# Kernel tuning notes

Measured on AMD Instinct MI355X. Metric: run time of the kernel, lower is better.

## Reference

```python
import math
import jax, jax.numpy as jnp
import numpy as np

B, FEAT, H, W = 4, 256, 48, 48
NH = 8
PE = 10            # pe_dim -> 3*PE = 30 positional channels
DK = FEAT // NH    # 32
DV = FEAT // NH    # 32
SCALE = 2.0 * math.pi
TEMPERATURE = 10000.0
BN_EPS = 1e-5


def pos_en_sine(h, w, num_pos_feats=PE):
    """3-axis sine positional encoding (y, x, and a constant 'o' axis) -> [3*PE, h, w]."""
    eps = 1e-6
    ones = jnp.ones((h, w), jnp.float32)
    y_embed = jnp.cumsum(ones, axis=0)
    x_embed = jnp.cumsum(ones, axis=1)
    y_embed = y_embed / (y_embed[-1:, :] + eps) * SCALE
    x_embed = x_embed / (x_embed[:, -1:] + eps) * SCALE
    o_embed = ones * SCALE  # third axis, constant when no explicit pos is given
    dim_t = jnp.arange(num_pos_feats, dtype=jnp.float32)
    dim_t = TEMPERATURE ** (2.0 * jnp.floor(dim_t / 2.0) / num_pos_feats)

    def enc(e):  # e: [h, w] -> [h, w, PE] interleaved sin/cos
        p = e[..., None] / dim_t
        return jnp.stack([jnp.sin(p[..., 0::2]), jnp.cos(p[..., 1::2])], axis=-1).reshape(h, w, num_pos_feats)

    pe = jnp.concatenate([enc(y_embed), enc(x_embed), enc(o_embed)], axis=-1)  # [h, w, 3*PE]
    return jnp.transpose(pe, (2, 0, 1))  # [3*PE, h, w]


def conv1x1(w, x):  # w: [out_c, in_c], x: [b, in_c, h, w]
    return jnp.einsum('oc,bchw->bohw', w, x)


def setup_inputs() -> dict:
    key = jax.random.key(0)
    ks = jax.random.split(key, 16)
    s = 0.02
    return {
        'q': jax.random.normal(ks[0], (B, FEAT, H, W), jnp.float32),
        'k': jax.random.normal(ks[1], (B, FEAT, H, W), jnp.float32),
        'v': jax.random.normal(ks[2], (B, FEAT, H, W), jnp.float32),
        'wq': jax.random.normal(ks[3], (NH * DK, FEAT + 3 * PE), jnp.float32) * s,
        'wk': jax.random.normal(ks[4], (NH * DK, FEAT + 3 * PE), jnp.float32) * s,
        'wv': jax.random.normal(ks[5], (NH * DV, FEAT), jnp.float32) * s,
        'wfc': jax.random.normal(ks[6], (FEAT, NH * DV), jnp.float32) * s,
        'w1': jax.random.normal(ks[7], (FEAT, FEAT), jnp.float32) * s,
        'b1': jnp.zeros((FEAT,), jnp.float32),
        'w2': jax.random.normal(ks[8], (FEAT, FEAT), jnp.float32) * s,
        'b2': jnp.zeros((FEAT,), jnp.float32),
        'gamma': jnp.ones((FEAT,), jnp.float32),
        'beta': jnp.zeros((FEAT,), jnp.float32),
    }


def reference(q, k, v, wq, wk, wv, wfc, w1, b1, w2, b2, gamma, beta):
    b, c, h, w = q.shape
    n = h * w
    pe = pos_en_sine(h, w)                                # [3*PE, h, w]
    peb = jnp.broadcast_to(pe[None], (b,) + pe.shape)
    qc = jnp.concatenate([q, peb], axis=1)                # [b, FEAT+30, h, w]
    kc = jnp.concatenate([k, peb], axis=1)
    # multi-head softmax attention over all spatial tokens
    Q = conv1x1(wq, qc).reshape(b, NH, DK, n)             # [b, nh, dk, n]
    K = conv1x1(wk, kc).reshape(b, NH, DK, n)
    V = conv1x1(wv, v).reshape(b, NH, DV, n)
    scores = jnp.einsum('bhdn,bhdm->bhnm', Q, K) / jnp.sqrt(jnp.float32(DK))
    attn = jax.nn.softmax(scores, axis=-1)                # [b, nh, n, n]
    O = jnp.einsum('bhnm,bhdm->bhdn', attn, V).reshape(b, NH * DV, h, w)
    O = conv1x1(wfc, O)                                   # [b, FEAT, h, w]
    # pointwise FFN + residual
    h1 = jax.nn.relu(conv1x1(w1, O) + b1[None, :, None, None])
    h2 = conv1x1(w2, h1) + b2[None, :, None, None]
    out = O + h2
    # BatchNorm2d (training mode: batch statistics over (b, h, w), biased var)
    mean = jnp.mean(out, axis=(0, 2, 3), keepdims=True)
    var = jnp.var(out, axis=(0, 2, 3), keepdims=True)
    out = (out - mean) / jnp.sqrt(var + BN_EPS)
    out = out * gamma[None, :, None, None] + beta[None, :, None, None]
    return out
```

## Files before the change

### kernel.cpp

```cpp
#include <hip/hip_runtime.h>
#include <hip/hip_bf16.h>

#define NTOK 2304

typedef short  short8  __attribute__((ext_vector_type(8)));
typedef unsigned short ushort8v __attribute__((ext_vector_type(8)));
typedef float  f32x4   __attribute__((ext_vector_type(4)));

static __device__ __forceinline__ unsigned short f2bfu(float f){
  __hip_bfloat16 h = __float2bfloat16(f);
  union { __hip_bfloat16 h; unsigned short u; } cv; cv.h = h; return cv.u;
}

static __device__ __forceinline__ void plane32(unsigned &a, unsigned &b){
  asm("v_permlane32_swap_b32 %0, %1" : "+v"(a), "+v"(b));
}
static __device__ __forceinline__ void plane16(unsigned &a, unsigned &b){
  asm("v_permlane16_swap_b32 %0, %1" : "+v"(a), "+v"(b));
}
static __device__ __forceinline__ short8 xpose_p(f32x4 sa, f32x4 sb){
  unsigned x0, x1, y0, y1;
  asm("v_cvt_pk_bf16_f32 %0, %1, %2" : "=v"(x0) : "v"(sa[0]), "v"(sa[1]));
  asm("v_cvt_pk_bf16_f32 %0, %1, %2" : "=v"(x1) : "v"(sa[2]), "v"(sa[3]));
  asm("v_cvt_pk_bf16_f32 %0, %1, %2" : "=v"(y0) : "v"(sb[0]), "v"(sb[1]));
  asm("v_cvt_pk_bf16_f32 %0, %1, %2" : "=v"(y1) : "v"(sb[2]), "v"(sb[3]));
  plane32(x0, y0);
  plane32(x1, y1);
  plane16(x0, y0);
  plane16(x1, y1);
  union { unsigned u[4]; short8 s; } r;
  r.u[0] = x0; r.u[1] = x1; r.u[2] = y0; r.u[3] = y1;
  return r.s;
}


__global__ void trip_kernel(float* out, int n){
  int i = blockIdx.x*256 + threadIdx.x;
  if (i < n) out[i] = 1000.0f;
}

__global__ __launch_bounds__(256) void setup_kernel(
    const float* __restrict__ q, const float* __restrict__ k,
    const float* __restrict__ v,
    const float* __restrict__ wq, const float* __restrict__ wk,
    const float* __restrict__ wv, const float* __restrict__ wfc,
    const float* __restrict__ w1, const float* __restrict__ w2,
    unsigned short* __restrict__ qT, unsigned short* __restrict__ kT,
    unsigned short* __restrict__ vT,
    unsigned short* __restrict__ wqp, unsigned short* __restrict__ wkp,
    unsigned short* __restrict__ wvb, unsigned short* __restrict__ wfcb,
    unsigned short* __restrict__ w1b, unsigned short* __restrict__ w2b,
    float* __restrict__ bns){
  const int bid = blockIdx.x;
  const int t = threadIdx.x;
  __shared__ __align__(16) unsigned short tile[64*72];

  if (bid < 1728){
    if (bid == 0){ bns[t] = 0.f; bns[256+t] = 0.f; }
    const int x = bid % 36, rem = bid / 36;
    const int y = rem % 4, z = rem / 4;
    const int tz = z >> 2, b = z & 3;
    const float* src = (tz==0) ? q : ((tz==1) ? k : v);
    unsigned short* dst = (tz==0) ? qT : ((tz==1) ? kT : vT);
    const int W = (tz==2) ? 256 : 288;
    const int n0 = x*64, c0 = y*64;
    const int jj = t & 7, cl = t >> 3;
    #pragma unroll
    for (int p=0; p<2; p++){
      int c = c0 + 32*p + cl;
      const float* s = src + (size_t)(b*256 + c)*NTOK + n0 + 8*jj;
      float4 f0 = *(const float4*)s;
      float4 f1 = *(const float4*)(s + 4);
      unsigned short* tr = tile + 32*p + cl;
      tr[(8*jj+0)*72] = f2bfu(f0.x); tr[(8*jj+1)*72] = f2bfu(f0.y);
      tr[(8*jj+2)*72] = f2bfu(f0.z); tr[(8*jj+3)*72] = f2bfu(f0.w);
      tr[(8*jj+4)*72] = f2bfu(f1.x); tr[(8*jj+5)*72] = f2bfu(f1.y);
      tr[(8*jj+6)*72] = f2bfu(f1.z); tr[(8*jj+7)*72] = f2bfu(f1.w);
    }
    __syncthreads();
    #pragma unroll
    for (int p=0; p<2; p++){
      int nl = 32*p + cl;
      ushort8v val = *(const ushort8v*)(tile + nl*72 + 8*jj);
      *(ushort8v*)(dst + (size_t)(b*2304 + n0 + nl)*W + c0 + 8*jj) = val;
    }
  } else if (bid < 1800){
    const int id2 = bid - 1728;
    const int x = id2 % 9, yy = id2 / 9;
    const int n = x*256 + t;
    unsigned short* buf = (yy < 4) ? qT : kT;
    const int b = yy & 3;
    const int i = n / 48, j = n - 48*i;
    const float k2pi = 6.283185307179586f;
    const float f = k2pi / 48.000001f;
    float ey = (float)(i+1) * f;
    float ex = (float)(j+1) * f;
    unsigned short u[32];
    #pragma unroll
    for (int p=0; p<10; p++){
      float inv = exp2f(-2.6575424759098898f * (float)(p >> 1));
      float vy = ey*inv, vx = ex*inv, vo = k2pi*inv;
      u[p]    = f2bfu((p&1) ? cosf(vy) : sinf(vy));
      u[10+p] = f2bfu((p&1) ? cosf(vx) : sinf(vx));
      u[20+p] = f2bfu((p&1) ? cosf(vo) : sinf(vo));
    }
    u[30] = 0; u[31] = 0;
    unsigned short* dst = buf + (size_t)(b*2304 + n)*288 + 256;
    #pragma unroll
    for (int m=0; m<4; m++) *(ushort8v*)(dst + 8*m) = *(const ushort8v*)(u + 8*m);
  } else if (bid < 2376){
    const int id3 = bid - 1800;
    const int x = id3 % 288, y = id3 / 288;
    const int idx = x*256 + t;
    const float* src = y ? wk : wq;
    unsigned short* dst = y ? wkp : wqp;
    const float scale = y ? 1.f : 0.25503486f;
    int row = idx / 288, col = idx - row*288;
    dst[idx] = (col < 286) ? f2bfu(src[row*286 + col] * scale) : (unsigned short)0;
  } else {
    const int id4 = bid - 2376;
    const int x = id4 % 256, y = id4 / 256;
    const int idx = x*256 + t;
    const float* src = (y==0)?wv:((y==1)?wfc:((y==2)?w1:w2));
    unsigned short* dst = (y==0)?wvb:((y==1)?wfcb:((y==2)?w1b:w2b));
    dst[idx] = f2bfu(src[idx]);
  }
}

template<int KSTEPS>
static __device__ __forceinline__ void gemm_core(
    const unsigned short* __restrict__ arow,
    const unsigned short* __restrict__ wrow, int wstride, f32x4* acc){
  #pragma unroll
  for (int kk=0; kk<KSTEPS; kk++){
    short8 af = *(const short8*)(arow + 32*kk);
    #pragma unroll
    for (int to=0; to<2; to++){
      short8 bf = *(const short8*)(wrow + (size_t)(16*to)*wstride + 32*kk);
      acc[to] = __builtin_amdgcn_mfma_f32_16x16x32_bf16(af, bf, acc[to], 0,0,0);
    }
  }
}

static __device__ __forceinline__ void epi_tok(
    const f32x4* acc, unsigned short* __restrict__ out_tok,
    int b, int tok, int n0, int lane, int quad, int cc,
    unsigned short* __restrict__ tlw){
  #pragma unroll
  for (int to=0; to<2; to++)
    #pragma unroll
    for (int r=0; r<4; r++)
      tlw[(4*quad + r)*40 + 16*to + cc] = f2bfu(acc[to][r]);
  const int row = lane & 15, ch = lane >> 4;
  ushort8v val = *(const ushort8v*)(tlw + row*40 + 8*ch);
  *(ushort8v*)(out_tok + (size_t)(b*2304 + tok + row)*256 + n0 + 8*ch) = val;
}

static __device__ __forceinline__ void epi_chan(
    const f32x4* acc, unsigned short* __restrict__ out_chan,
    int b, int tok, int n0, int quad, int cc){
  #pragma unroll
  for (int to=0; to<2; to++){
    ushort4 pk;
    pk.x = f2bfu(acc[to][0]); pk.y = f2bfu(acc[to][1]);
    pk.z = f2bfu(acc[to][2]); pk.w = f2bfu(acc[to][3]);
    *(ushort4*)(out_chan + (size_t)(b*256 + n0 + 16*to + cc)*NTOK + tok + 4*quad) = pk;
  }
}

__global__ __launch_bounds__(256) void qkv_kernel(
    const unsigned short* __restrict__ qT, const unsigned short* __restrict__ kT,
    const unsigned short* __restrict__ vT,
    const unsigned short* __restrict__ wqp, const unsigned short* __restrict__ wkp,
    const unsigned short* __restrict__ wvb,
    unsigned short* __restrict__ Qt, unsigned short* __restrict__ Kt,
    unsigned short* __restrict__ V2){
  const int t = threadIdx.x;
  const int w = t >> 6, lane = t & 63;
  const int quad = lane >> 4, cc = lane & 15;
  const int t0 = blockIdx.x*64, n0 = blockIdx.y*32;
  const int tz = blockIdx.z >> 2, b = blockIdx.z & 3;
  const int tok = t0 + 16*w;
  __shared__ __align__(16) unsigned short tl[4*16*40];
  unsigned short* tlw = tl + w*640;

  f32x4 acc[2];
  acc[0] = (f32x4){0.f,0.f,0.f,0.f}; acc[1] = acc[0];

  if (tz == 0){
    const unsigned short* arow = qT + (size_t)(b*2304 + tok + cc)*288 + 8*quad;
    const unsigned short* wrow = wqp + (size_t)(n0 + cc)*288 + 8*quad;
    gemm_core<9>(arow, wrow, 288, acc);
    epi_tok(acc, Qt, b, tok, n0, lane, quad, cc, tlw);
  } else if (tz == 1){
    const unsigned short* arow = kT + (size_t)(b*2304 + tok + cc)*288 + 8*quad;
    const unsigned short* wrow = wkp + (size_t)(n0 + cc)*288 + 8*quad;
    gemm_core<9>(arow, wrow, 288, acc);
    epi_tok(acc, Kt, b, tok, n0, lane, quad, cc, tlw);
  } else {
    const unsigned short* arow = vT + (size_t)(b*2304 + tok + cc)*256 + 8*quad;
    const unsigned short* wrow = wvb + (size_t)(n0 + cc)*256 + 8*quad;
    gemm_core<8>(arow, wrow, 256, acc);
    epi_chan(acc, V2, b, tok, n0, quad, cc);
  }
}

template<int EPI>
__global__ __launch_bounds__(256) void gemm2_kernel(
    const unsigned short* __restrict__ aT,
    const unsigned short* __restrict__ wgt,
    const float* __restrict__ bias,
    unsigned short* __restrict__ out_tok,
    unsigned short* __restrict__ out_chan,
    const unsigned short* __restrict__ resid,
    float* __restrict__ pre_out, float* __restrict__ bns, int relu){
  const int t = threadIdx.x;
  const int w = t >> 6, lane = t & 63;
  const int quad = lane >> 4, cc = lane & 15;
  const int t0 = blockIdx.x*64, n0 = blockIdx.y*32, b = blockIdx.z;
  const int tok = t0 + 16*w;
  __shared__ __align__(16) unsigned short tl[4*16*40];
  unsigned short* tlw = tl + w*640;

  const unsigned short* arow = aT + (size_t)(b*2304 + tok + cc)*256 + 8*quad;
  const unsigned short* wrow = wgt + (size_t)(n0 + cc)*256 + 8*quad;
  f32x4 acc[2];
  acc[0] = (f32x4){0.f,0.f,0.f,0.f}; acc[1] = acc[0];
  gemm_core<8>(arow, wrow, 256, acc);

  if (bias){
    #pragma unroll
    for (int to=0; to<2; to++){
      float bv = bias[n0 + 16*to + cc];
      #pragma unroll
      for (int r=0; r<4; r++) acc[to][r] += bv;
    }
  }
  if (relu){
    #pragma unroll
    for (int to=0; to<2; to++)
      #pragma unroll
      for (int r=0; r<4; r++) acc[to][r] = fmaxf(acc[to][r], 0.f);
  }

  if (EPI == 2){
    epi_chan(acc, out_chan, b, tok, n0, quad, cc);
    epi_tok(acc, out_tok, b, tok, n0, lane, quad, cc, tlw);
  }
  if (EPI == 0){
    epi_tok(acc, out_tok, b, tok, n0, lane, quad, cc, tlw);
  }
  if (EPI == 3){
    #pragma unroll
    for (int to=0; to<2; to++){
      size_t co = (size_t)(b*256 + n0 + 16*to + cc)*NTOK + tok + 4*quad;
      ushort4 rr = *(const ushort4*)(resid + co);
      float p0 = acc[to][0] + __uint_as_float((unsigned)rr.x << 16);
      float p1 = acc[to][1] + __uint_as_float((unsigned)rr.y << 16);
      float p2 = acc[to][2] + __uint_as_float((unsigned)rr.z << 16);
      float p3 = acc[to][3] + __uint_as_float((unsigned)rr.w << 16);
      *(float4*)(pre_out + co) = make_float4(p0,p1,p2,p3);
      float s1 = (p0+p1)+(p2+p3);
      float s2 = (p0*p0+p1*p1)+(p2*p2+p3*p3);
      s1 += __shfl_xor(s1, 16, 64); s1 += __shfl_xor(s1, 32, 64);
      s2 += __shfl_xor(s2, 16, 64); s2 += __shfl_xor(s2, 32, 64);
      if (quad == 0){
        atomicAdd(&bns[n0 + 16*to + cc],       s1);
        atomicAdd(&bns[256 + n0 + 16*to + cc], s2);
      }
    }
  }
}

__global__ __launch_bounds__(256) void attn_kernel(
    const unsigned short* __restrict__ Qt, const unsigned short* __restrict__ Kt,
    const unsigned short* __restrict__ V2, unsigned short* __restrict__ AO){
  const int t = threadIdx.x;
  const int w = t >> 6, lane = t & 63;
  const int quad = lane >> 4, cc = lane & 15;
  const int h = blockIdx.y, b = blockIdx.z;
  const int q0 = blockIdx.x*64;

  const unsigned short* qb = Qt + (size_t)(b*2304 + q0 + cc)*256 + h*32 + 8*quad;
  short8 qf0 = *(const short8*)(qb);
  short8 qf1 = *(const short8*)(qb + 16*256);
  short8 qf2 = *(const short8*)(qb + 32*256);
  short8 qf3 = *(const short8*)(qb + 48*256);

  const unsigned short* kb = Kt + (size_t)(b*2304 + cc)*256 + h*32 + 8*quad;
  const unsigned short* vb = V2 + (size_t)(b*256 + h*32 + cc)*NTOK + 8*quad;

  __shared__ __align__(16) float mg_lds[4*2112];

  f32x4 o00={0.f,0.f,0.f,0.f}, o10=o00, o01=o00, o11=o00;
  f32x4 o02=o00, o12=o00, o03=o00, o13=o00;
  float lsum0=0.f, lsum1=0.f, lsum2=0.f, lsum3=0.f;

  const int kstart = w*576;
  short8 kf0 = *(const short8*)(kb + (size_t)kstart*256);
  short8 kf1 = *(const short8*)(kb + (size_t)(kstart+16)*256);
  short8 vf0 = *(const short8*)(vb + kstart);
  short8 vf1 = *(const short8*)(vb + (size_t)16*NTOK + kstart);

  #pragma unroll 1
  for (int it = 0; it < 18; ++it){
    const int ko = kstart + it*32;
    const int rk = (it < 17) ? ko + 32 : kstart;
    const f32x4 z = {0.f,0.f,0.f,0.f};

    f32x4 s00 = __builtin_amdgcn_mfma_f32_16x16x32_bf16(kf0, qf0, z, 0,0,0);
    f32x4 s10 = __builtin_amdgcn_mfma_f32_16x16x32_bf16(kf1, qf0, z, 0,0,0);
    f32x4 s01 = __builtin_amdgcn_mfma_f32_16x16x32_bf16(kf0, qf1, z, 0,0,0);
    f32x4 s11 = __builtin_amdgcn_mfma_f32_16x16x32_bf16(kf1, qf1, z, 0,0,0);
    f32x4 s02 = __builtin_amdgcn_mfma_f32_16x16x32_bf16(kf0, qf2, z, 0,0,0);
    f32x4 s12 = __builtin_amdgcn_mfma_f32_16x16x32_bf16(kf1, qf2, z, 0,0,0);
    f32x4 s03 = __builtin_amdgcn_mfma_f32_16x16x32_bf16(kf0, qf3, z, 0,0,0);
    f32x4 s13 = __builtin_amdgcn_mfma_f32_16x16x32_bf16(kf1, qf3, z, 0,0,0);
    kf0 = *(const short8*)(kb + (size_t)rk*256);
    kf1 = *(const short8*)(kb + (size_t)(rk+16)*256);

    #pragma unroll
    for (int r=0; r<4; r++){
      s00[r] = __builtin_amdgcn_exp2f(s00[r]);
      s10[r] = __builtin_amdgcn_exp2f(s10[r]);
      s01[r] = __builtin_amdgcn_exp2f(s01[r]);
      s11[r] = __builtin_amdgcn_exp2f(s11[r]);
      s02[r] = __builtin_amdgcn_exp2f(s02[r]);
      s12[r] = __builtin_amdgcn_exp2f(s12[r]);
      s03[r] = __builtin_amdgcn_exp2f(s03[r]);
      s13[r] = __builtin_amdgcn_exp2f(s13[r]);
    }
    lsum0 += ((s00[0]+s00[1])+(s00[2]+s00[3])) + ((s10[0]+s10[1])+(s10[2]+s10[3]));
    lsum1 += ((s01[0]+s01[1])+(s01[2]+s01[3])) + ((s11[0]+s11[1])+(s11[2]+s11[3]));
    lsum2 += ((s02[0]+s02[1])+(s02[2]+s02[3])) + ((s12[0]+s12[1])+(s12[2]+s12[3]));
    lsum3 += ((s03[0]+s03[1])+(s03[2]+s03[3])) + ((s13[0]+s13[1])+(s13[2]+s13[3]));

    short8 pf0 = xpose_p(s00, s10);
    short8 pf1 = xpose_p(s01, s11);
    short8 pf2 = xpose_p(s02, s12);
    short8 pf3 = xpose_p(s03, s13);

    o00 = __builtin_amdgcn_mfma_f32_16x16x32_bf16(vf0, pf0, o00, 0,0,0);
    o10 = __builtin_amdgcn_mfma_f32_16x16x32_bf16(vf1, pf0, o10, 0,0,0);
    o01 = __builtin_amdgcn_mfma_f32_16x16x32_bf16(vf0, pf1, o01, 0,0,0);
    o11 = __builtin_amdgcn_mfma_f32_16x16x32_bf16(vf1, pf1, o11, 0,0,0);
    o02 = __builtin_amdgcn_mfma_f32_16x16x32_bf16(vf0, pf2, o02, 0,0,0);
    o12 = __builtin_amdgcn_mfma_f32_16x16x32_bf16(vf1, pf2, o12, 0,0,0);
    o03 = __builtin_amdgcn_mfma_f32_16x16x32_bf16(vf0, pf3, o03, 0,0,0);
    o13 = __builtin_amdgcn_mfma_f32_16x16x32_bf16(vf1, pf3, o13, 0,0,0);
    vf0 = *(const short8*)(vb + rk);
    vf1 = *(const short8*)(vb + (size_t)16*NTOK + rk);
  }

  lsum0 += __shfl_xor(lsum0, 16, 64); lsum0 += __shfl_xor(lsum0, 32, 64);
  lsum1 += __shfl_xor(lsum1, 16, 64); lsum1 += __shfl_xor(lsum1, 32, 64);
  lsum2 += __shfl_xor(lsum2, 16, 64); lsum2 += __shfl_xor(lsum2, 32, 64);
  lsum3 += __shfl_xor(lsum3, 16, 64); lsum3 += __shfl_xor(lsum3, 32, 64);

  float* mg = mg_lds + w*2112;
  #pragma unroll
  for (int i=0;i<4;i++){
    mg[(0*8 + 0*4 + i)*64 + lane] = o00[i];
    mg[(0*8 + 1*4 + i)*64 + lane] = o10[i];
    mg[(1*8 + 0*4 + i)*64 + lane] = o01[i];
    mg[(1*8 + 1*4 + i)*64 + lane] = o11[i];
    mg[(2*8 + 0*4 + i)*64 + lane] = o02[i];
    mg[(2*8 + 1*4 + i)*64 + lane] = o12[i];
    mg[(3*8 + 0*4 + i)*64 + lane] = o03[i];
    mg[(3*8 + 1*4 + i)*64 + lane] = o13[i];
  }
  if (quad == 0){
    mg[2048 +  0 + cc] = lsum0;
    mg[2048 + 16 + cc] = lsum1;
    mg[2048 + 32 + cc] = lsum2;
    mg[2048 + 48 + cc] = lsum3;
  }
  __syncthreads();

  const float* m0 = mg_lds;
  const float* m1 = mg_lds + 2112;
  const float* m2 = mg_lds + 4224;
  const float* m3 = mg_lds + 6336;
  const int la = 2048 + w*16 + cc;
  float ls = (m0[la] + m1[la]) + (m2[la] + m3[la]);
  float inv = 1.f / ls;

  float r0, r1, r2, r3, r4, r5, r6, r7;
  {
    int a0 = (w*8 + 0)*64 + lane;
    r0 = (m0[a0] + m1[a0]) + (m2[a0] + m3[a0]);
    int a1 = (w*8 + 1)*64 + lane;
    r1 = (m0[a1] + m1[a1]) + (m2[a1] + m3[a1]);
    int a2 = (w*8 + 2)*64 + lane;
    r2 = (m0[a2] + m1[a2]) + (m2[a2] + m3[a2]);
    int a3 = (w*8 + 3)*64 + lane;
    r3 = (m0[a3] + m1[a3]) + (m2[a3] + m3[a3]);
    int a4 = (w*8 + 4)*64 + lane;
    r4 = (m0[a4] + m1[a4]) + (m2[a4] + m3[a4]);
    int a5 = (w*8 + 5)*64 + lane;
    r5 = (m0[a5] + m1[a5]) + (m2[a5] + m3[a5]);
    int a6 = (w*8 + 6)*64 + lane;
    r6 = (m0[a6] + m1[a6]) + (m2[a6] + m3[a6]);
    int a7 = (w*8 + 7)*64 + lane;
    r7 = (m0[a7] + m1[a7]) + (m2[a7] + m3[a7]);
  }

  const int qcol = q0 + w*16 + cc;
  unsigned short* dst = AO + (size_t)(b*2304 + qcol)*256 + h*32 + 4*quad;
  ushort4 p0;
  p0.x = f2bfu(r0*inv); p0.y = f2bfu(r1*inv);
  p0.z = f2bfu(r2*inv); p0.w = f2bfu(r3*inv);
  *(ushort4*)(dst) = p0;
  ushort4 p1;
  p1.x = f2bfu(r4*inv); p1.y = f2bfu(r5*inv);
  p1.z = f2bfu(r6*inv); p1.w = f2bfu(r7*inv);
  *(ushort4*)(dst + 16) = p1;
}

__global__ __launch_bounds__(256) void bn_final_kernel(
    const float* __restrict__ pre, const float* __restrict__ bns,
    const float* __restrict__ g, const float* __restrict__ bt,
    float* __restrict__ out){
  int i0 = (blockIdx.x*256 + threadIdx.x)*4;
  int ch = (i0 / NTOK) & 255;
  float mean = bns[ch] * (1.f/9216.f);
  float var  = bns[256+ch] * (1.f/9216.f) - mean*mean;
  float scl = g[ch] * rsqrtf(fmaxf(var, 0.f) + 1e-5f);
  float sh  = bt[ch] - mean*scl;
  float4 x = *(const float4*)(pre + i0);
  *(float4*)(out + i0) = make_float4(x.x*scl+sh, x.y*scl+sh, x.z*scl+sh, x.w*scl+sh);
}

extern "C" void kernel_launch(void* const* d_in, const int* in_sizes, int n_in,
                              void* d_out, int out_size, void* d_ws, size_t ws_size,
                              hipStream_t stream){
  const size_t NEED = 2112 + (size_t)15155200*2;
  if (ws_size < NEED){
    trip_kernel<<<dim3((out_size+255)/256), dim3(256), 0, stream>>>((float*)d_out, out_size);
    return;
  }
  const float* q   = (const float*)d_in[0];
  const float* k   = (const float*)d_in[1];
  const float* v   = (const float*)d_in[2];
  const float* wq  = (const float*)d_in[3];
  const float* wk  = (const float*)d_in[4];
  const float* wv  = (const float*)d_in[5];
  const float* wfc = (const float*)d_in[6];
  const float* w1  = (const float*)d_in[7];
  const float* b1  = (const float*)d_in[8];
  const float* w2  = (const float*)d_in[9];
  const float* b2  = (const float*)d_in[10];
  const float* gm  = (const float*)d_in[11];
  const float* bt  = (const float*)d_in[12];

  float* ws  = (float*)d_ws;
  float* bns = ws;
  unsigned short* ub = (unsigned short*)(ws + 528);
  unsigned short* u_qT = ub;
  unsigned short* u_kT = ub + 2654208;
  unsigned short* u_vT = ub + 5308416;
  unsigned short* u_Qt = ub + 7667712;
  unsigned short* u_Kt = ub + 10027008;
  unsigned short* u_V2 = ub + 12386304;
  unsigned short* wqp  = ub + 14745600;
  unsigned short* wkp  = ub + 14819328;
  unsigned short* wvb  = ub + 14893056;
  unsigned short* wfcb = ub + 14958592;
  unsigned short* w1b  = ub + 15024128;
  unsigned short* w2b  = ub + 15089664;
  unsigned short* AO  = u_qT;
  unsigned short* h1  = u_kT;
  unsigned short* Ofc = u_vT;
  unsigned short* Oc  = u_Qt;
  float* pre = (float*)(u_Kt);

  setup_kernel<<<dim3(3400), dim3(256), 0, stream>>>(
      q, k, v, wq, wk, wv, wfc, w1, w2,
      u_qT, u_kT, u_vT, wqp, wkp, wvb, wfcb, w1b, w2b, bns);

  qkv_kernel<<<dim3(36,8,12), dim3(256), 0, stream>>>(u_qT, u_kT, u_vT, wqp, wkp, wvb, u_Qt, u_Kt, u_V2);

  attn_kernel<<<dim3(36,8,4), dim3(256), 0, stream>>>(u_Qt, u_Kt, u_V2, AO);

  gemm2_kernel<2><<<dim3(36,8,4), dim3(256), 0, stream>>>(AO,  wfcb, nullptr, Ofc, Oc, nullptr, nullptr, nullptr, 0);
  gemm2_kernel<0><<<dim3(36,8,4), dim3(256), 0, stream>>>(Ofc, w1b,  b1,      h1,  nullptr, nullptr, nullptr, nullptr, 1);
  gemm2_kernel<3><<<dim3(36,8,4), dim3(256), 0, stream>>>(h1,  w2b,  b2,      nullptr, nullptr, Oc, pre, bns, 0);

  bn_final_kernel<<<dim3(2304), dim3(256), 0, stream>>>(pre, bns, gm, bt, (float*)d_out);
}
```

Baseline: 248.4 us.

## Fuse output projection, FFN and residual into a single LDS-staged kernel

Replaces the three separate GEMM launches (output projection, FFN layer 1 with ReLU, FFN layer 2 with residual and BN stats) with one kernel. Each block processes 16 tokens across all 256 channels and keeps intermediate activations in shared memory. This is meant to remove the global-memory round trips of the intermediates and two kernel launches. In exchange, each block re-reads all three weight matrices from L2/global, the grid has fewer blocks, and the residual now uses fp32 accumulators instead of a bf16-rounded copy.

```diff
diff --git a/kernel.cpp b/kernel.cpp
--- a/kernel.cpp
+++ b/kernel.cpp
@@ -205,69 +205,92 @@
   }
 }
 
-template<int EPI>
-__global__ __launch_bounds__(256) void gemm2_kernel(
-    const unsigned short* __restrict__ aT,
-    const unsigned short* __restrict__ wgt,
-    const float* __restrict__ bias,
-    unsigned short* __restrict__ out_tok,
-    unsigned short* __restrict__ out_chan,
-    const unsigned short* __restrict__ resid,
-    float* __restrict__ pre_out, float* __restrict__ bns, int relu){
+__global__ __launch_bounds__(256) void ffn_kernel(
+    const unsigned short* __restrict__ AO,
+    const unsigned short* __restrict__ wfcb,
+    const unsigned short* __restrict__ w1b,
+    const unsigned short* __restrict__ w2b,
+    const float* __restrict__ b1, const float* __restrict__ b2,
+    float* __restrict__ pre_out, float* __restrict__ bns){
   const int t = threadIdx.x;
   const int w = t >> 6, lane = t & 63;
   const int quad = lane >> 4, cc = lane & 15;
-  const int t0 = blockIdx.x*64, n0 = blockIdx.y*32, b = blockIdx.z;
-  const int tok = t0 + 16*w;
-  __shared__ __align__(16) unsigned short tl[4*16*40];
-  unsigned short* tlw = tl + w*640;
-
-  const unsigned short* arow = aT + (size_t)(b*2304 + tok + cc)*256 + 8*quad;
-  const unsigned short* wrow = wgt + (size_t)(n0 + cc)*256 + 8*quad;
-  f32x4 acc[2];
-  acc[0] = (f32x4){0.f,0.f,0.f,0.f}; acc[1] = acc[0];
-  gemm_core<8>(arow, wrow, 256, acc);
-
-  if (bias){
-    #pragma unroll
-    for (int to=0; to<2; to++){
-      float bv = bias[n0 + 16*to + cc];
-      #pragma unroll
-      for (int r=0; r<4; r++) acc[to][r] += bv;
-    }
-  }
-  if (relu){
-    #pragma unroll
-    for (int to=0; to<2; to++)
-      #pragma unroll
-      for (int r=0; r<4; r++) acc[to][r] = fmaxf(acc[to][r], 0.f);
-  }
-
-  if (EPI == 2){
-    epi_chan(acc, out_chan, b, tok, n0, quad, cc);
-    epi_tok(acc, out_tok, b, tok, n0, lane, quad, cc, tlw);
-  }
-  if (EPI == 0){
-    epi_tok(acc, out_tok, b, tok, n0, lane, quad, cc, tlw);
-  }
-  if (EPI == 3){
-    #pragma unroll
-    for (int to=0; to<2; to++){
-      size_t co = (size_t)(b*256 + n0 + 16*to + cc)*NTOK + tok + 4*quad;
-      ushort4 rr = *(const ushort4*)(resid + co);
-      float p0 = acc[to][0] + __uint_as_float((unsigned)rr.x << 16);
-      float p1 = acc[to][1] + __uint_as_float((unsigned)rr.y << 16);
-      float p2 = acc[to][2] + __uint_as_float((unsigned)rr.z << 16);
-      float p3 = acc[to][3] + __uint_as_float((unsigned)rr.w << 16);
-      *(float4*)(pre_out + co) = make_float4(p0,p1,p2,p3);
-      float s1 = (p0+p1)+(p2+p3);
-      float s2 = (p0*p0+p1*p1)+(p2*p2+p3*p3);
-      s1 += __shfl_xor(s1, 16, 64); s1 += __shfl_xor(s1, 32, 64);
-      s2 += __shfl_xor(s2, 16, 64); s2 += __shfl_xor(s2, 32, 64);
-      if (quad == 0){
-        atomicAdd(&bns[n0 + 16*to + cc],       s1);
-        atomicAdd(&bns[256 + n0 + 16*to + cc], s2);
-      }
+  const int tok0 = blockIdx.x * 16;
+  const int b = blockIdx.y;
+  const int ocb = 64 * w;
+
+  __shared__ __align__(16) unsigned short T0[16*264];
+  __shared__ __align__(16) unsigned short T1[16*264];
+
+  const unsigned short* arow = AO + (size_t)(b*2304 + tok0 + cc)*256 + 8*quad;
+  f32x4 acc1[4];
+  acc1[0] = (f32x4){0.f,0.f,0.f,0.f}; acc1[1]=acc1[0]; acc1[2]=acc1[0]; acc1[3]=acc1[0];
+  #pragma unroll
+  for (int kk=0; kk<8; kk++){
+    short8 af = *(const short8*)(arow + 32*kk);
+    #pragma unroll
+    for (int of=0; of<4; of++){
+      short8 bf = *(const short8*)(wfcb + (size_t)(ocb + 16*of + cc)*256 + 8*quad + 32*kk);
+      acc1[of] = __builtin_amdgcn_mfma_f32_16x16x32_bf16(af, bf, acc1[of], 0,0,0);
+    }
+  }
+  #pragma unroll
+  for (int of=0; of<4; of++)
+    #pragma unroll
+    for (int r=0; r<4; r++)
+      T0[(4*quad + r)*264 + ocb + 16*of + cc] = f2bfu(acc1[of][r]);
+  __syncthreads();
+
+  f32x4 acc2[4];
+  acc2[0] = (f32x4){0.f,0.f,0.f,0.f}; acc2[1]=acc2[0]; acc2[2]=acc2[0]; acc2[3]=acc2[0];
+  #pragma unroll
+  for (int kk=0; kk<8; kk++){
+    short8 af = *(const short8*)(T0 + cc*264 + 8*quad + 32*kk);
+    #pragma unroll
+    for (int of=0; of<4; of++){
+      short8 bf = *(const short8*)(w1b + (size_t)(ocb + 16*of + cc)*256 + 8*quad + 32*kk);
+      acc2[of] = __builtin_amdgcn_mfma_f32_16x16x32_bf16(af, bf, acc2[of], 0,0,0);
+    }
+  }
+  #pragma unroll
+  for (int of=0; of<4; of++){
+    float bv = b1[ocb + 16*of + cc];
+    #pragma unroll
+    for (int r=0; r<4; r++){
+      float hv = fmaxf(acc2[of][r] + bv, 0.f);
+      T1[(4*quad + r)*264 + ocb + 16*of + cc] = f2bfu(hv);
+    }
+  }
+  __syncthreads();
+
+  f32x4 acc3[4];
+  acc3[0] = (f32x4){0.f,0.f,0.f,0.f}; acc3[1]=acc3[0]; acc3[2]=acc3[0]; acc3[3]=acc3[0];
+  #pragma unroll
+  for (int kk=0; kk<8; kk++){
+    short8 af = *(const short8*)(T1 + cc*264 + 8*quad + 32*kk);
+    #pragma unroll
+    for (int of=0; of<4; of++){
+      short8 bf = *(const short8*)(w2b + (size_t)(ocb + 16*of + cc)*256 + 8*quad + 32*kk);
+      acc3[of] = __builtin_amdgcn_mfma_f32_16x16x32_bf16(af, bf, acc3[of], 0,0,0);
+    }
+  }
+  #pragma unroll
+  for (int of=0; of<4; of++){
+    const int oc = ocb + 16*of + cc;
+    float bv = b2[oc];
+    float p0 = acc3[of][0] + bv + acc1[of][0];
+    float p1 = acc3[of][1] + bv + acc1[of][1];
+    float p2 = acc3[of][2] + bv + acc1[of][2];
+    float p3 = acc3[of][3] + bv + acc1[of][3];
+    *(float4*)(pre_out + (size_t)(b*256 + oc)*NTOK + tok0 + 4*quad) =
+        make_float4(p0, p1, p2, p3);
+    float s1 = (p0+p1)+(p2+p3);
+    float s2 = (p0*p0+p1*p1)+(p2*p2+p3*p3);
+    s1 += __shfl_xor(s1, 16, 64); s1 += __shfl_xor(s1, 32, 64);
+    s2 += __shfl_xor(s2, 16, 64); s2 += __shfl_xor(s2, 32, 64);
+    if (quad == 0){
+      atomicAdd(&bns[oc],       s1);
+      atomicAdd(&bns[256 + oc], s2);
     }
   }
 }
@@ -469,9 +492,6 @@
   unsigned short* w1b  = ub + 15024128;
   unsigned short* w2b  = ub + 15089664;
   unsigned short* AO  = u_qT;
-  unsigned short* h1  = u_kT;
-  unsigned short* Ofc = u_vT;
-  unsigned short* Oc  = u_Qt;
   float* pre = (float*)(u_Kt);
 
   setup_kernel<<<dim3(3400), dim3(256), 0, stream>>>(
@@ -482,9 +502,7 @@
 
   attn_kernel<<<dim3(36,8,4), dim3(256), 0, stream>>>(u_Qt, u_Kt, u_V2, AO);
 
-  gemm2_kernel<2><<<dim3(36,8,4), dim3(256), 0, stream>>>(AO,  wfcb, nullptr, Ofc, Oc, nullptr, nullptr, nullptr, 0);
-  gemm2_kernel<0><<<dim3(36,8,4), dim3(256), 0, stream>>>(Ofc, w1b,  b1,      h1,  nullptr, nullptr, nullptr, nullptr, 1);
-  gemm2_kernel<3><<<dim3(36,8,4), dim3(256), 0, stream>>>(h1,  w2b,  b2,      nullptr, nullptr, Oc, pre, bns, 0);
+  ffn_kernel<<<dim3(144,4), dim3(256), 0, stream>>>(AO, wfcb, w1b, w2b, b1, b2, pre, bns);
 
   bn_final_kernel<<<dim3(2304), dim3(256), 0, stream>>>(pre, bns, gm, bt, (float*)d_out);
 }
```

After: 230.6 us. -7.1%, faster.
